# Kernel optimization log

Measured on AMD Instinct MI355X. Metric: run time of the kernel, lower is better.

Reference implementation:

```python
import jax, jax.numpy as jnp
import numpy as np

IN_FEATURES = 1024
OUT_FEATURES = 128


def setup_inputs() -> dict:
    key = jax.random.key(0)
    k1, k2, k3, k4, k5 = jax.random.split(key, 5)
    B, T, E, D = 4, 4096, IN_FEATURES, OUT_FEATURES
    s_in = 1.0 / np.sqrt(E)
    s_d = 1.0 / np.sqrt(D)
    return {
        "x": jax.random.normal(k1, (B, T, E), dtype=jnp.float32),
        "Wk": jax.random.uniform(k2, (E, D), jnp.float32, -s_in, s_in),
        "Wq": jax.random.uniform(k3, (E, D), jnp.float32, -s_in, s_in),
        "Wv": jax.random.uniform(k4, (E, D), jnp.float32, -s_in, s_in),
        "Wp": jax.random.uniform(k5, (D, D), jnp.float32, -s_d, s_d),
    }


def reference(x, Wk, Wq, Wv, Wp):
    # x: [B, T, E]; projections stored as [in, out] (torch Linear transposed)
    B, T, E = x.shape
    D = Wk.shape[1]
    k = x @ Wk  # [B, T, D]
    q = x @ Wq
    v = x @ Wv
    scale = 1.0 / jnp.sqrt(jnp.asarray(D, x.dtype))
    attn = jnp.einsum("btd,bsd->bts", q, k) * scale  # [B, T, T]
    causal = jnp.tril(jnp.ones((T, T), dtype=bool))
    attn = jnp.where(causal, attn, -jnp.inf)
    attn = jax.nn.softmax(attn, axis=-1)
    out = jnp.einsum("bts,bsd->btd", attn, v)  # [B, T, D]
    return out @ Wp  # dropout p=0.0 -> identity
```

## Files before the change

### kernel.cpp

```cpp
#include <hip/hip_runtime.h>

#define E_DIM 1024
#define D_DIM 128
#define T_DIM 4096

typedef unsigned short u16;
typedef u16 u16x8 __attribute__((ext_vector_type(8)));
typedef u16 u16x4 __attribute__((ext_vector_type(4)));
typedef __bf16 bf16x8 __attribute__((ext_vector_type(8)));
typedef float f32x4 __attribute__((ext_vector_type(4)));

__device__ __forceinline__ u16 cvt_bf16(float f) {
    unsigned u = __float_as_uint(f);
    u += 0x7FFF + ((u >> 16) & 1);
    return (u16)(u >> 16);
}

__device__ __forceinline__ float bf2f(u16 v) {
    return __uint_as_float(((unsigned)v) << 16);
}

__device__ __forceinline__ f32x4 mfma16(u16x8 a, u16x8 b, f32x4 c) {
    return __builtin_amdgcn_mfma_f32_16x16x32_bf16(
        __builtin_bit_cast(bf16x8, a), __builtin_bit_cast(bf16x8, b), c, 0, 0, 0);
}

__device__ __forceinline__ void gld_lds16(const void* g, void* l) {
    __builtin_amdgcn_global_load_lds(
        (const __attribute__((address_space(1))) unsigned int*)g,
        (__attribute__((address_space(3))) unsigned int*)l, 16, 0, 0);
}

__global__ void prep_kernel(const float* __restrict__ Wk, const float* __restrict__ Wq,
                            const float* __restrict__ Wv, const float* __restrict__ Wp,
                            u16* __restrict__ Wqt, u16* __restrict__ Wkt,
                            u16* __restrict__ Wvt, u16* __restrict__ Wpt) {
    int tid = blockIdx.x * 256 + threadIdx.x;
    const int WT = 128 * 1024;
    if (tid < 3 * WT) {
        int w = tid / WT;
        int r = tid - w * WT;
        int n = r >> 10, k = r & 1023;
        const float* W = (w == 0) ? Wq : (w == 1) ? Wk : Wv;
        u16* Wt = (w == 0) ? Wqt : (w == 1) ? Wkt : Wvt;
        Wt[r] = cvt_bf16(W[k * 128 + n]);
    } else {
        int r = tid - 3 * WT;
        if (r < 128 * 128) {
            int n = r >> 7, k = r & 127;
            Wpt[r] = cvt_bf16(Wp[k * 128 + n]);
        }
    }
}

__global__ __launch_bounds__(256) void qkv_kernel(
        const float* __restrict__ x,
        const u16* __restrict__ Wqt, const u16* __restrict__ Wkt, const u16* __restrict__ Wvt,
        u16* __restrict__ qb, u16* __restrict__ kb, u16* __restrict__ vT) {
    __shared__ __align__(16) char smem[24576];

    const int t = threadIdx.x;
    const int w = t >> 6;
    const int lane = t & 63;
    const int lr = lane & 15;
    const int lg = lane >> 4;
    const int m = w & 1;
    const int n = w >> 1;
    const int rg = blockIdx.x >> 1;
    const int cgrp = blockIdx.x & 1;
    const int r0 = rg * 64;

    #define STAGE_W(K0, BUF) do {                                                 \
        char* wB_ = smem + (BUF) * 12288;                                         \
        _Pragma("unroll")                                                         \
        for (int c2 = 0; c2 < 3; ++c2) {                                          \
            const int rl_ = c2 * 64 + (t >> 2);                                   \
            const int gn_ = cgrp * 192 + rl_;                                     \
            const u16* W_ = (gn_ < 128) ? Wqt : (gn_ < 256) ? Wkt : Wvt;          \
            const int s_ = ((t & 3) - (rl_ >> 1)) & 3;                            \
            gld_lds16(W_ + (size_t)(gn_ & 127) * E_DIM + (K0) + 8 * s_,           \
                      wB_ + c2 * 4096 + t * 16);                                  \
        }                                                                         \
    } while (0)

    const float* xp0 = x + (size_t)(r0 + 32 * m + lr) * E_DIM + lg * 8;
    const float* xp1 = xp0 + 16 * E_DIM;

    float4 xr[2][2];
    #define XLOAD(K0) do {                                                        \
        xr[0][0] = *(const float4*)(xp0 + (K0));                                  \
        xr[0][1] = *(const float4*)(xp0 + (K0) + 4);                              \
        xr[1][0] = *(const float4*)(xp1 + (K0));                                  \
        xr[1][1] = *(const float4*)(xp1 + (K0) + 4);                              \
    } while (0)

    f32x4 acc[2][6];
    #pragma unroll
    for (int i = 0; i < 2; ++i)
        #pragma unroll
        for (int j = 0; j < 6; ++j) acc[i][j] = f32x4{0.f, 0.f, 0.f, 0.f};

    XLOAD(0);
    STAGE_W(0, 0);
    asm volatile("s_waitcnt vmcnt(0)" ::: "memory");
    __syncthreads();

    int buf = 0;
    for (int k0 = 0; k0 < E_DIM; k0 += 32) {
        if (k0 + 32 < E_DIM) STAGE_W(k0 + 32, buf ^ 1);

        u16x8 av[2];
        #pragma unroll
        for (int i = 0; i < 2; ++i) {
            av[i][0] = cvt_bf16(xr[i][0].x); av[i][1] = cvt_bf16(xr[i][0].y);
            av[i][2] = cvt_bf16(xr[i][0].z); av[i][3] = cvt_bf16(xr[i][0].w);
            av[i][4] = cvt_bf16(xr[i][1].x); av[i][5] = cvt_bf16(xr[i][1].y);
            av[i][6] = cvt_bf16(xr[i][1].z); av[i][7] = cvt_bf16(xr[i][1].w);
        }
        if (k0 + 32 < E_DIM) XLOAD(k0 + 32);

        char* wB = smem + buf * 12288;
        __builtin_amdgcn_s_setprio(1);
        #pragma unroll
        for (int nt = 0; nt < 6; ++nt) {
            const int ln = n * 96 + nt * 16 + lr;
            u16x8 bv = *(u16x8*)(wB + ln * 64 + (((lg + (ln >> 1)) & 3) << 4));
            acc[0][nt] = mfma16(av[0], bv, acc[0][nt]);
            acc[1][nt] = mfma16(av[1], bv, acc[1][nt]);
        }
        __builtin_amdgcn_s_setprio(0);

        asm volatile("s_waitcnt vmcnt(0)" ::: "memory");
        __syncthreads();
        buf ^= 1;
    }
    #undef STAGE_W
    #undef XLOAD

    const int bb = r0 >> 12;
    #pragma unroll
    for (int i = 0; i < 2; ++i) {
        const int row0 = r0 + 32 * m + 16 * i + 4 * lg;
        const int tt0 = row0 & 4095;
        #pragma unroll
        for (int nt = 0; nt < 6; ++nt) {
            const int col_g = cgrp * 192 + n * 96 + nt * 16 + lr;
            const int j = col_g >> 7;
            const int colw = col_g & 127;
            if (j < 2) {
                u16* outb = (j == 0) ? qb : kb;
                #pragma unroll
                for (int reg = 0; reg < 4; ++reg)
                    outb[(size_t)(row0 + reg) * D_DIM + colw] = cvt_bf16(acc[i][nt][reg]);
            } else {
                u16x4 pv;
                #pragma unroll
                for (int reg = 0; reg < 4; ++reg) pv[reg] = cvt_bf16(acc[i][nt][reg]);
                *(u16x4*)&vT[((size_t)(bb * 128 + colw)) * T_DIM + tt0] = pv;
            }
        }
    }
}

__global__ __launch_bounds__(512) void attn_kernel(
        const u16* __restrict__ qb, const u16* __restrict__ kb, const u16* __restrict__ vT,
        u16* __restrict__ Opart, float* __restrict__ ml, int SPLIT) {
    const int g = blockIdx.x;
    const int b = blockIdx.y;
    int i, c;
    if (SPLIT) {
        int k = 0;
        while (2 * (k + 1) * (k + 2) <= g) ++k;
        const int off = g - 2 * k * (k + 1);
        const int iband = off / (k + 1);
        c = off - iband * (k + 1);
        i = 4 * k + iband;
    } else { i = g; c = 0; }

    const int q0 = i * 128;
    const int kv_beg = c * 512;
    const int kv_end = SPLIT ? min(q0 + 128, kv_beg + 512) : (q0 + 128);
    const int slot = b * gridDim.x + g;

    __shared__ __align__(16) char smem[81920];

    const int t = threadIdx.x;
    const int w = t >> 6;
    const int lane = t & 63;
    const int lr = lane & 15;
    const int lg = lane >> 4;
    const size_t base = (size_t)b * T_DIM * D_DIM;

    u16x8 qf[4];
    {
        const u16* qp = qb + base + (size_t)(q0 + 16 * w + lr) * D_DIM + lg * 8;
        #pragma unroll
        for (int dk = 0; dk < 4; ++dk) qf[dk] = *(const u16x8*)(qp + dk * 32);
    }

    const char* kpb = (const char*)(kb + base);
    const char* vpb = (const char*)(vT + (size_t)b * D_DIM * T_DIM);
    const int key = (lr & 7) << 4;

    #define STAGE(S0, BUF) do {                                                   \
        char* kB_ = smem + (BUF) * 16384;                                         \
        char* vB_ = smem + 32768 + (BUF) * 16384;                                 \
        const int wbase_ = (t >> 6) * 1024;                                       \
        _Pragma("unroll")                                                         \
        for (int c2 = 0; c2 < 2; ++c2) {                                          \
            const int krow_ = c2 * 32 + (t >> 4);                                 \
            gld_lds16(kpb + (size_t)((S0) + krow_) * 256 +                        \
                      (((t & 15) * 16) ^ ((krow_ & 7) * 16)),                     \
                      kB_ + c2 * 8192 + wbase_);                                  \
            const int vrow_ = c2 * 64 + (t >> 3);                                 \
            gld_lds16(vpb + (size_t)vrow_ * (T_DIM * 2) + (size_t)(S0) * 2 +      \
                      (((t & 7) * 16) ^ ((vrow_ & 7) * 16)),                      \
                      vB_ + c2 * 8192 + wbase_);                                  \
        }                                                                         \
    } while (0)

    f32x4 oacc[8];
    #pragma unroll
    for (int nn = 0; nn < 8; ++nn) oacc[nn] = f32x4{0.f, 0.f, 0.f, 0.f};
    float m_run = -1e30f, l_run = 0.f;
    const float scale2 = 0.12752048520120164f;
    const int qrow = q0 + 16 * w + lr;

    STAGE(kv_beg, 0);
    asm volatile("s_waitcnt vmcnt(0)" ::: "memory");
    __syncthreads();

    int buf = 0;
    for (int s0 = kv_beg; s0 < kv_end; s0 += 64) {
        if (s0 + 64 < kv_end) STAGE(s0 + 64, buf ^ 1);

        char* kB  = smem + buf * 16384;
        char* vB  = smem + 32768 + buf * 16384;
        char* psB = smem + 65536 + w * 2048;

        f32x4 sacc[4];
        #pragma unroll
        for (int nn = 0; nn < 4; ++nn) sacc[nn] = f32x4{0.f, 0.f, 0.f, 0.f};
        __builtin_amdgcn_s_setprio(1);
        #pragma unroll
        for (int dk = 0; dk < 4; ++dk) {
            #pragma unroll
            for (int nt = 0; nt < 4; ++nt) {
                u16x8 kfr = *(u16x8*)(kB + (nt * 16 + lr) * 256 + ((dk * 64 + lg * 16) ^ key));
                sacc[nt] = mfma16(kfr, qf[dk], sacc[nt]);
            }
        }
        __builtin_amdgcn_s_setprio(0);

        float sv[4][4];
        const bool need_mask = (s0 + 63 > q0 + 16 * w);
        #pragma unroll
        for (int nt = 0; nt < 4; ++nt) {
            #pragma unroll
            for (int r = 0; r < 4; ++r) {
                float v = sacc[nt][r] * scale2;
                if (need_mask && (s0 + nt * 16 + 4 * lg + r) > qrow) v = -1e30f;
                sv[nt][r] = v;
            }
        }

        float tmax = sv[0][0];
        #pragma unroll
        for (int nt = 0; nt < 4; ++nt)
            #pragma unroll
            for (int r = 0; r < 4; ++r) tmax = fmaxf(tmax, sv[nt][r]);
        tmax = fmaxf(tmax, __shfl_xor(tmax, 16));
        tmax = fmaxf(tmax, __shfl_xor(tmax, 32));
        float m_new = fmaxf(m_run, tmax);
        float rsc = __builtin_amdgcn_exp2f(m_run - m_new);
        m_run = m_new;
        float tsum = 0.f;
        #pragma unroll
        for (int nt = 0; nt < 4; ++nt)
            #pragma unroll
            for (int r = 0; r < 4; ++r) {
                sv[nt][r] = __builtin_amdgcn_exp2f(sv[nt][r] - m_new);
                tsum += sv[nt][r];
            }
        tsum += __shfl_xor(tsum, 16);
        tsum += __shfl_xor(tsum, 32);
        l_run = l_run * rsc + tsum;

        #pragma unroll
        for (int nt = 0; nt < 8; ++nt)
            #pragma unroll
            for (int r = 0; r < 4; ++r) oacc[nt][r] *= rsc;

        #pragma unroll
        for (int nt = 0; nt < 4; ++nt) {
            u16x4 pv4;
            #pragma unroll
            for (int r = 0; r < 4; ++r) pv4[r] = cvt_bf16(sv[nt][r]);
            *(u16x4*)(psB + lr * 128 + ((nt * 32 + lg * 8) ^ key)) = pv4;
        }

        u16x8 pA0 = *(u16x8*)(psB + lr * 128 + ((lg * 16) ^ key));
        u16x8 pA1 = *(u16x8*)(psB + lr * 128 + ((64 + lg * 16) ^ key));

        __builtin_amdgcn_s_setprio(1);
        #pragma unroll
        for (int nt = 0; nt < 8; ++nt) {
            u16x8 bv0 = *(u16x8*)(vB + (nt * 16 + lr) * 128 + ((lg * 16) ^ key));
            oacc[nt] = mfma16(bv0, pA0, oacc[nt]);
            u16x8 bv1 = *(u16x8*)(vB + (nt * 16 + lr) * 128 + ((64 + lg * 16) ^ key));
            oacc[nt] = mfma16(bv1, pA1, oacc[nt]);
        }
        __builtin_amdgcn_s_setprio(0);

        asm volatile("s_waitcnt vmcnt(0)" ::: "memory");
        __syncthreads();
        buf ^= 1;
    }
    #undef STAGE

    if (lg == 0) {
        int row = 16 * w + lr;
        ml[(size_t)(slot * 128 + row) * 2]     = m_run;
        ml[(size_t)(slot * 128 + row) * 2 + 1] = l_run;
    }

    const float invl = 1.f / l_run;
    const int orw = 16 * w + lr;
    #pragma unroll
    for (int nt = 0; nt < 8; ++nt) {
        u16x4 ov;
        #pragma unroll
        for (int r = 0; r < 4; ++r) ov[r] = cvt_bf16(oacc[nt][r] * invl);
        *(u16x4*)(smem + orw * 256 + ((32 * nt + 8 * lg) ^ ((orw & 7) << 4))) = ov;
    }
    __syncthreads();
    u16* op = Opart + (size_t)slot * 16384;
    const int orow = t >> 2;
    const int oseg = t & 3;
    #pragma unroll
    for (int j = 0; j < 4; ++j) {
        u16x8 vv = *(u16x8*)(smem + orow * 256 + ((oseg * 64 + j * 16) ^ ((orow & 7) << 4)));
        *(u16x8*)(op + orow * 128 + oseg * 32 + j * 8) = vv;
    }
}

__global__ __launch_bounds__(256) void combine_kernel(
        const u16* __restrict__ Opart, const float* __restrict__ ml,
        const u16* __restrict__ Wpt, float* __restrict__ out,
        int SPLIT, int NSLOT) {
    const int io = blockIdx.x;
    const int b = blockIdx.y;
    const int i = io >> 1;
    const int half = io & 1;
    int NC, g0;
    if (SPLIT) {
        int k = i >> 2;
        NC = k + 1;
        g0 = 2 * k * (k + 1) + (i & 3) * (k + 1);
    } else { NC = 1; g0 = i; }
    const int slot0 = b * NSLOT + g0;

    __shared__ u16 Os[64][136];
    const int t = threadIdx.x;
    const int row = t >> 2, seg = (t & 3) * 32;
    const int row_in = half * 64 + row;

    float m_fin = -1e30f;
    for (int c = 0; c < NC; ++c)
        m_fin = fmaxf(m_fin, ml[(size_t)((slot0 + c) * 128 + row_in) * 2]);

    float acc[32];
    #pragma unroll
    for (int j = 0; j < 32; ++j) acc[j] = 0.f;
    float l_fin = 0.f;
    for (int c = 0; c < NC; ++c) {
        float mcv = ml[(size_t)((slot0 + c) * 128 + row_in) * 2];
        float lcv = ml[(size_t)((slot0 + c) * 128 + row_in) * 2 + 1];
        float wgt = __builtin_amdgcn_exp2f(mcv - m_fin) * lcv;
        l_fin += wgt;
        const u16* opc = Opart + (size_t)(slot0 + c) * 16384 + row_in * 128 + seg;
        #pragma unroll
        for (int j = 0; j < 4; ++j) {
            u16x8 v = *(const u16x8*)(opc + j * 8);
            #pragma unroll
            for (int e = 0; e < 8; ++e)
                acc[j * 8 + e] += bf2f(v[e]) * wgt;
        }
    }
    const float inv = 1.f / l_fin;

    #pragma unroll
    for (int j = 0; j < 4; ++j) {
        u16x8 ov;
        #pragma unroll
        for (int e = 0; e < 8; ++e) ov[e] = cvt_bf16(acc[j * 8 + e] * inv);
        *(u16x8*)&Os[row][seg + j * 8] = ov;
    }
    __syncthreads();

    const int w = t >> 6;
    const int lane = t & 63;
    const int lr = lane & 15;
    const int lg = lane >> 4;
    u16x8 af[4];
    #pragma unroll
    for (int dk = 0; dk < 4; ++dk)
        af[dk] = *(u16x8*)&Os[16 * w + lr][dk * 32 + lg * 8];
    float* op = out + ((size_t)b * T_DIM + io * 64) * D_DIM;
    #pragma unroll
    for (int nt = 0; nt < 8; ++nt) {
        f32x4 y = f32x4{0.f, 0.f, 0.f, 0.f};
        #pragma unroll
        for (int dk = 0; dk < 4; ++dk) {
            u16x8 bv = *(const u16x8*)&Wpt[(size_t)(nt * 16 + lr) * D_DIM + dk * 32 + lg * 8];
            y = mfma16(af[dk], bv, y);
        }
        #pragma unroll
        for (int r = 0; r < 4; ++r)
            op[(size_t)(16 * w + 4 * lg + r) * D_DIM + nt * 16 + lr] = y[r];
    }
}

extern "C" void kernel_launch(void* const* d_in, const int* in_sizes, int n_in,
                              void* d_out, int out_size, void* d_ws, size_t ws_size,
                              hipStream_t stream) {
    const float* x  = (const float*)d_in[0];
    const float* Wk = (const float*)d_in[1];
    const float* Wq = (const float*)d_in[2];
    const float* Wv = (const float*)d_in[3];
    const float* Wp = (const float*)d_in[4];
    float* out = (float*)d_out;

    char* ws = (char*)d_ws;
    u16* qb  = (u16*)(ws);
    u16* kb  = (u16*)(ws + 4194304);
    u16* vT  = (u16*)(ws + 8388608);
    u16* Wqt = (u16*)(ws + 12582912);
    u16* Wkt = (u16*)(ws + 12582912 + 262144);
    u16* Wvt = (u16*)(ws + 12582912 + 524288);
    u16* Wpt = (u16*)(ws + 12582912 + 786432);
    float* ml   = (float*)(ws + 13631488);
    u16* Opart  = (u16*)(ws + 14680064);

    const bool big = ws_size >= (size_t)36 * 1024 * 1024;
    const int SPLIT = big ? 1 : 0;
    const int GX = big ? 144 : 32;

    prep_kernel<<<1600, 256, 0, stream>>>(Wk, Wq, Wv, Wp, Wqt, Wkt, Wvt, Wpt);
    qkv_kernel<<<512, 256, 0, stream>>>(x, Wqt, Wkt, Wvt, qb, kb, vT);
    attn_kernel<<<dim3(GX, 4), 512, 0, stream>>>(qb, kb, vT, Opart, ml, SPLIT);
    combine_kernel<<<dim3(64, 4), 256, 0, stream>>>(Opart, ml, Wpt, out, SPLIT, GX);
}
```

Baseline: 106.2 us.

## Double-buffer x register loads and unroll QKV projection loop by two

```diff
diff --git a/kernel.cpp b/kernel.cpp
--- a/kernel.cpp
+++ b/kernel.cpp
@@ -86,56 +86,81 @@
     const float* xp0 = x + (size_t)(r0 + 32 * m + lr) * E_DIM + lg * 8;
     const float* xp1 = xp0 + 16 * E_DIM;
 
-    float4 xr[2][2];
-    #define XLOAD(K0) do {                                                        \
-        xr[0][0] = *(const float4*)(xp0 + (K0));                                  \
-        xr[0][1] = *(const float4*)(xp0 + (K0) + 4);                              \
-        xr[1][0] = *(const float4*)(xp1 + (K0));                                  \
-        xr[1][1] = *(const float4*)(xp1 + (K0) + 4);                              \
+    float4 xa[4], xb[4];
+    #define XLOAD(arr, K0) do {                                                   \
+        arr[0] = *(const float4*)(xp0 + (K0));                                    \
+        arr[1] = *(const float4*)(xp0 + (K0) + 4);                                \
+        arr[2] = *(const float4*)(xp1 + (K0));                                    \
+        arr[3] = *(const float4*)(xp1 + (K0) + 4);                                \
     } while (0)
 
+    #define CVT_AV(av, arr) do {                                                  \
+        _Pragma("unroll")                                                         \
+        for (int i = 0; i < 2; ++i) {                                             \
+            av[i][0] = cvt_bf16(arr[2*i].x);   av[i][1] = cvt_bf16(arr[2*i].y);   \
+            av[i][2] = cvt_bf16(arr[2*i].z);   av[i][3] = cvt_bf16(arr[2*i].w);   \
+            av[i][4] = cvt_bf16(arr[2*i+1].x); av[i][5] = cvt_bf16(arr[2*i+1].y); \
+            av[i][6] = cvt_bf16(arr[2*i+1].z); av[i][7] = cvt_bf16(arr[2*i+1].w); \
+        }                                                                         \
+    } while (0)
+
+    #define MFMA_PHASE(BUF, av) do {                                              \
+        char* wB = smem + (BUF) * 12288;                                          \
+        __builtin_amdgcn_s_setprio(1);                                            \
+        _Pragma("unroll")                                                         \
+        for (int nt = 0; nt < 6; ++nt) {                                          \
+            const int ln = n * 96 + nt * 16 + lr;                                 \
+            u16x8 bv = *(u16x8*)(wB + ln * 64 + (((lg + (ln >> 1)) & 3) << 4));   \
+            acc[0][nt] = mfma16(av[0], bv, acc[0][nt]);                           \
+            acc[1][nt] = mfma16(av[1], bv, acc[1][nt]);                           \
+        }                                                                         \
+        __builtin_amdgcn_s_setprio(0);                                            \
+    } while (0)
+
     f32x4 acc[2][6];
     #pragma unroll
     for (int i = 0; i < 2; ++i)
         #pragma unroll
         for (int j = 0; j < 6; ++j) acc[i][j] = f32x4{0.f, 0.f, 0.f, 0.f};
 
-    XLOAD(0);
+    XLOAD(xa, 0);
+    XLOAD(xb, 32);
     STAGE_W(0, 0);
     asm volatile("s_waitcnt vmcnt(0)" ::: "memory");
-    __syncthreads();
-
-    int buf = 0;
-    for (int k0 = 0; k0 < E_DIM; k0 += 32) {
-        if (k0 + 32 < E_DIM) STAGE_W(k0 + 32, buf ^ 1);
-
-        u16x8 av[2];
-        #pragma unroll
-        for (int i = 0; i < 2; ++i) {
-            av[i][0] = cvt_bf16(xr[i][0].x); av[i][1] = cvt_bf16(xr[i][0].y);
-            av[i][2] = cvt_bf16(xr[i][0].z); av[i][3] = cvt_bf16(xr[i][0].w);
-            av[i][4] = cvt_bf16(xr[i][1].x); av[i][5] = cvt_bf16(xr[i][1].y);
-            av[i][6] = cvt_bf16(xr[i][1].z); av[i][7] = cvt_bf16(xr[i][1].w);
-        }
-        if (k0 + 32 < E_DIM) XLOAD(k0 + 32);
-
-        char* wB = smem + buf * 12288;
-        __builtin_amdgcn_s_setprio(1);
-        #pragma unroll
-        for (int nt = 0; nt < 6; ++nt) {
-            const int ln = n * 96 + nt * 16 + lr;
-            u16x8 bv = *(u16x8*)(wB + ln * 64 + (((lg + (ln >> 1)) & 3) << 4));
-            acc[0][nt] = mfma16(av[0], bv, acc[0][nt]);
-            acc[1][nt] = mfma16(av[1], bv, acc[1][nt]);
-        }
-        __builtin_amdgcn_s_setprio(0);
-
-        asm volatile("s_waitcnt vmcnt(0)" ::: "memory");
-        __syncthreads();
-        buf ^= 1;
+    __builtin_amdgcn_s_barrier();
+
+    for (int kk = 0; kk < 16; ++kk) {
+        const int k0 = kk * 64;
+        const bool more = (kk < 15);
+        u16x8 avA[2];
+        CVT_AV(avA, xa);
+        __builtin_amdgcn_sched_barrier(0);
+        STAGE_W(k0 + 32, 1);
+        __builtin_amdgcn_sched_barrier(0);
+        if (more) XLOAD(xa, k0 + 64);
+        __builtin_amdgcn_sched_barrier(0);
+        MFMA_PHASE(0, avA);
+        if (more) asm volatile("s_waitcnt vmcnt(4) lgkmcnt(0)" ::: "memory");
+        else      asm volatile("s_waitcnt vmcnt(0) lgkmcnt(0)" ::: "memory");
+        __builtin_amdgcn_s_barrier();
+        u16x8 avB[2];
+        CVT_AV(avB, xb);
+        __builtin_amdgcn_sched_barrier(0);
+        if (more) {
+            STAGE_W(k0 + 64, 0);
+            __builtin_amdgcn_sched_barrier(0);
+            XLOAD(xb, k0 + 96);
+        }
+        __builtin_amdgcn_sched_barrier(0);
+        MFMA_PHASE(1, avB);
+        if (more) asm volatile("s_waitcnt vmcnt(4) lgkmcnt(0)" ::: "memory");
+        else      asm volatile("s_waitcnt vmcnt(0) lgkmcnt(0)" ::: "memory");
+        __builtin_amdgcn_s_barrier();
     }
     #undef STAGE_W
     #undef XLOAD
+    #undef CVT_AV
+    #undef MFMA_PHASE
 
     const int bb = r0 >> 12;
     #pragma unroll
```

Result: no change. 108.0 us (+1.7%).

## Restructure QKV projection into 64x384 tiles with 4-stage weight pipeline

Applied to the files above, without the earlier changes.

```diff
diff --git a/kernel.cpp b/kernel.cpp
--- a/kernel.cpp
+++ b/kernel.cpp
@@ -53,111 +53,113 @@
     }
 }
 
-__global__ __launch_bounds__(256) void qkv_kernel(
+__global__ __launch_bounds__(512) void qkv_kernel(
         const float* __restrict__ x,
         const u16* __restrict__ Wqt, const u16* __restrict__ Wkt, const u16* __restrict__ Wvt,
         u16* __restrict__ qb, u16* __restrict__ kb, u16* __restrict__ vT) {
-    __shared__ __align__(16) char smem[24576];
+    __shared__ __align__(16) char smem[98304];
 
     const int t = threadIdx.x;
     const int w = t >> 6;
     const int lane = t & 63;
     const int lr = lane & 15;
     const int lg = lane >> 4;
-    const int m = w & 1;
-    const int n = w >> 1;
-    const int rg = blockIdx.x >> 1;
-    const int cgrp = blockIdx.x & 1;
-    const int r0 = rg * 64;
+    const int m4 = w & 3;
+    const int n2 = w >> 2;
+    const int r0 = blockIdx.x * 64;
 
     #define STAGE_W(K0, BUF) do {                                                 \
-        char* wB_ = smem + (BUF) * 12288;                                         \
+        char* wB_ = smem + (BUF) * 24576;                                         \
         _Pragma("unroll")                                                         \
         for (int c2 = 0; c2 < 3; ++c2) {                                          \
-            const int rl_ = c2 * 64 + (t >> 2);                                   \
-            const int gn_ = cgrp * 192 + rl_;                                     \
-            const u16* W_ = (gn_ < 128) ? Wqt : (gn_ < 256) ? Wkt : Wvt;          \
+            const int rl_ = c2 * 128 + (t >> 2);                                  \
+            const u16* W_ = (rl_ < 128) ? Wqt : (rl_ < 256) ? Wkt : Wvt;          \
             const int s_ = ((t & 3) - (rl_ >> 1)) & 3;                            \
-            gld_lds16(W_ + (size_t)(gn_ & 127) * E_DIM + (K0) + 8 * s_,           \
-                      wB_ + c2 * 4096 + t * 16);                                  \
+            gld_lds16(W_ + (size_t)(rl_ & 127) * E_DIM + (K0) + 8 * s_,           \
+                      wB_ + c2 * 8192 + t * 16);                                  \
         }                                                                         \
     } while (0)
 
-    const float* xp0 = x + (size_t)(r0 + 32 * m + lr) * E_DIM + lg * 8;
-    const float* xp1 = xp0 + 16 * E_DIM;
-
-    float4 xr[2][2];
-    #define XLOAD(K0) do {                                                        \
-        xr[0][0] = *(const float4*)(xp0 + (K0));                                  \
-        xr[0][1] = *(const float4*)(xp0 + (K0) + 4);                              \
-        xr[1][0] = *(const float4*)(xp1 + (K0));                                  \
-        xr[1][1] = *(const float4*)(xp1 + (K0) + 4);                              \
+    const float* xp = x + (size_t)(r0 + 16 * m4 + lr) * E_DIM + lg * 8;
+
+    float4 xa[2], xb[2];
+    #define XLOAD(arr, K0) do {                                                   \
+        arr[0] = *(const float4*)(xp + (K0));                                     \
+        arr[1] = *(const float4*)(xp + (K0) + 4);                                 \
     } while (0)
 
-    f32x4 acc[2][6];
-    #pragma unroll
-    for (int i = 0; i < 2; ++i)
-        #pragma unroll
-        for (int j = 0; j < 6; ++j) acc[i][j] = f32x4{0.f, 0.f, 0.f, 0.f};
-
-    XLOAD(0);
+    #define CVT_AV(av, arr) do {                                                  \
+        av[0] = cvt_bf16(arr[0].x); av[1] = cvt_bf16(arr[0].y);                   \
+        av[2] = cvt_bf16(arr[0].z); av[3] = cvt_bf16(arr[0].w);                   \
+        av[4] = cvt_bf16(arr[1].x); av[5] = cvt_bf16(arr[1].y);                   \
+        av[6] = cvt_bf16(arr[1].z); av[7] = cvt_bf16(arr[1].w);                   \
+    } while (0)
+
+    f32x4 acc[12];
+    #pragma unroll
+    for (int j = 0; j < 12; ++j) acc[j] = f32x4{0.f, 0.f, 0.f, 0.f};
+
+    #define ITER(KK, XARR) do {                                                   \
+        const int kk_ = (KK);                                                     \
+        u16x8 av_;                                                                \
+        CVT_AV(av_, XARR);                                                        \
+        __builtin_amdgcn_sched_barrier(0);                                        \
+        if (kk_ < 30) {                                                           \
+            STAGE_W(kk_ * 32 + 64, (kk_ + 2) & 3);                                \
+            __builtin_amdgcn_sched_barrier(0);                                    \
+            XLOAD(XARR, kk_ * 32 + 64);                                           \
+        }                                                                         \
+        __builtin_amdgcn_sched_barrier(0);                                        \
+        {                                                                         \
+            char* wB = smem + ((kk_) & 3) * 24576;                                \
+            __builtin_amdgcn_s_setprio(1);                                        \
+            _Pragma("unroll")                                                     \
+            for (int nt = 0; nt < 12; ++nt) {                                     \
+                const int ln = n2 * 192 + nt * 16 + lr;                           \
+                u16x8 bv = *(u16x8*)(wB + ln * 64 + (((lg + (ln >> 1)) & 3) << 4)); \
+                acc[nt] = mfma16(av_, bv, acc[nt]);                               \
+            }                                                                     \
+            __builtin_amdgcn_s_setprio(0);                                        \
+        }                                                                         \
+        if (kk_ < 30) asm volatile("s_waitcnt vmcnt(5)" ::: "memory");            \
+        else          asm volatile("s_waitcnt vmcnt(0)" ::: "memory");            \
+        __builtin_amdgcn_s_barrier();                                             \
+    } while (0)
+
     STAGE_W(0, 0);
-    asm volatile("s_waitcnt vmcnt(0)" ::: "memory");
-    __syncthreads();
-
-    int buf = 0;
-    for (int k0 = 0; k0 < E_DIM; k0 += 32) {
-        if (k0 + 32 < E_DIM) STAGE_W(k0 + 32, buf ^ 1);
-
-        u16x8 av[2];
-        #pragma unroll
-        for (int i = 0; i < 2; ++i) {
-            av[i][0] = cvt_bf16(xr[i][0].x); av[i][1] = cvt_bf16(xr[i][0].y);
-            av[i][2] = cvt_bf16(xr[i][0].z); av[i][3] = cvt_bf16(xr[i][0].w);
-            av[i][4] = cvt_bf16(xr[i][1].x); av[i][5] = cvt_bf16(xr[i][1].y);
-            av[i][6] = cvt_bf16(xr[i][1].z); av[i][7] = cvt_bf16(xr[i][1].w);
-        }
-        if (k0 + 32 < E_DIM) XLOAD(k0 + 32);
-
-        char* wB = smem + buf * 12288;
-        __builtin_amdgcn_s_setprio(1);
-        #pragma unroll
-        for (int nt = 0; nt < 6; ++nt) {
-            const int ln = n * 96 + nt * 16 + lr;
-            u16x8 bv = *(u16x8*)(wB + ln * 64 + (((lg + (ln >> 1)) & 3) << 4));
-            acc[0][nt] = mfma16(av[0], bv, acc[0][nt]);
-            acc[1][nt] = mfma16(av[1], bv, acc[1][nt]);
-        }
-        __builtin_amdgcn_s_setprio(0);
-
-        asm volatile("s_waitcnt vmcnt(0)" ::: "memory");
-        __syncthreads();
-        buf ^= 1;
+    XLOAD(xa, 0);
+    STAGE_W(32, 1);
+    XLOAD(xb, 32);
+    asm volatile("s_waitcnt vmcnt(5)" ::: "memory");
+    __builtin_amdgcn_s_barrier();
+
+    for (int kk2 = 0; kk2 < 16; ++kk2) {
+        ITER(2 * kk2, xa);
+        ITER(2 * kk2 + 1, xb);
     }
     #undef STAGE_W
     #undef XLOAD
+    #undef CVT_AV
+    #undef ITER
 
     const int bb = r0 >> 12;
-    #pragma unroll
-    for (int i = 0; i < 2; ++i) {
-        const int row0 = r0 + 32 * m + 16 * i + 4 * lg;
-        const int tt0 = row0 & 4095;
-        #pragma unroll
-        for (int nt = 0; nt < 6; ++nt) {
-            const int col_g = cgrp * 192 + n * 96 + nt * 16 + lr;
-            const int j = col_g >> 7;
-            const int colw = col_g & 127;
-            if (j < 2) {
-                u16* outb = (j == 0) ? qb : kb;
-                #pragma unroll
-                for (int reg = 0; reg < 4; ++reg)
-                    outb[(size_t)(row0 + reg) * D_DIM + colw] = cvt_bf16(acc[i][nt][reg]);
-            } else {
-                u16x4 pv;
-                #pragma unroll
-                for (int reg = 0; reg < 4; ++reg) pv[reg] = cvt_bf16(acc[i][nt][reg]);
-                *(u16x4*)&vT[((size_t)(bb * 128 + colw)) * T_DIM + tt0] = pv;
-            }
+    const int row0 = r0 + 16 * m4 + 4 * lg;
+    const int tt0 = row0 & 4095;
+    #pragma unroll
+    for (int nt = 0; nt < 12; ++nt) {
+        const int col_g = n2 * 192 + nt * 16 + lr;
+        const int j = col_g >> 7;
+        const int colw = col_g & 127;
+        if (j < 2) {
+            u16* outb = (j == 0) ? qb : kb;
+            #pragma unroll
+            for (int reg = 0; reg < 4; ++reg)
+                outb[(size_t)(row0 + reg) * D_DIM + colw] = cvt_bf16(acc[nt][reg]);
+        } else {
+            u16x4 pv;
+            #pragma unroll
+            for (int reg = 0; reg < 4; ++reg) pv[reg] = cvt_bf16(acc[nt][reg]);
+            *(u16x4*)&vT[((size_t)(bb * 128 + colw)) * T_DIM + tt0] = pv;
         }
     }
 }
@@ -447,7 +449,7 @@
     const int GX = big ? 144 : 32;
 
     prep_kernel<<<1600, 256, 0, stream>>>(Wk, Wq, Wv, Wp, Wqt, Wkt, Wvt, Wpt);
-    qkv_kernel<<<512, 256, 0, stream>>>(x, Wqt, Wkt, Wvt, qb, kb, vT);
+    qkv_kernel<<<256, 512, 0, stream>>>(x, Wqt, Wkt, Wvt, qb, kb, vT);
     attn_kernel<<<dim3(GX, 4), 512, 0, stream>>>(qb, kb, vT, Opart, ml, SPLIT);
     combine_kernel<<<dim3(64, 4), 256, 0, stream>>>(Opart, ml, Wpt, out, SPLIT, GX);
 }
```

Result: faster. 94.74 us (-10.8%).
